# Kernel optimization log

Hardware: AMD Instinct MI355X
Metric: run time of the kernel (lower is better)

## Reference

```python
import jax, jax.numpy as jnp
import numpy as np

E = 1024
H = 4
N = 4096


def _l2norm(x, eps=1e-8):
    n = jnp.linalg.norm(x, axis=-1, keepdims=True)
    return x / jnp.maximum(n, eps)


def mha(q, k, v, in_w, in_b, out_w, out_b):
    # torch nn.MultiheadAttention, unbatched (L, E) inputs, H heads
    d = E // H
    qp = q @ in_w[:E].T + in_b[:E]            # [Lq, E]
    kp = k @ in_w[E:2 * E].T + in_b[E:2 * E]  # [Lk, E]
    vp = v @ in_w[2 * E:].T + in_b[2 * E:]    # [Lk, E]
    qh = qp.reshape(-1, H, d).transpose(1, 0, 2)  # [H, Lq, d]
    kh = kp.reshape(-1, H, d).transpose(1, 0, 2)
    vh = vp.reshape(-1, H, d).transpose(1, 0, 2)
    scores = jnp.einsum('hqd,hkd->hqk', qh, kh) / jnp.sqrt(jnp.asarray(d, qh.dtype))
    attn = jax.nn.softmax(scores, axis=-1)
    oh = jnp.einsum('hqk,hkd->hqd', attn, vh)     # [H, Lq, d]
    o = oh.transpose(1, 0, 2).reshape(-1, E)
    return o @ out_w.T + out_b


def setup_inputs() -> dict:
    key = jax.random.key(0)
    ks = jax.random.split(key, 20)
    f = lambda k, shape, s=1.0: jax.random.normal(k, shape, dtype=jnp.float32) * s
    inp = {
        'local_feat': _l2norm(f(ks[0], (N, E))),
        'global_feat': _l2norm(f(ks[1], (N, E))),
        'text_feat': _l2norm(f(ks[2], (N, E))),
        'pos_emb_local': f(ks[3], (E,), E ** -0.5),
        'pos_emb_global': f(ks[4], (E,), E ** -0.5),
        'fc_w': f(ks[5], (E, E), 0.02), 'fc_b': f(ks[6], (E,), 0.02),
        'lg_in_w': f(ks[7], (3 * E, E), 0.02), 'lg_in_b': f(ks[8], (3 * E,), 0.02),
        'lg_out_w': f(ks[9], (E, E), 0.02), 'lg_out_b': f(ks[10], (E,), 0.02),
        'vt_in_w': f(ks[11], (3 * E, E), 0.02), 'vt_in_b': f(ks[12], (3 * E,), 0.02),
        'vt_out_w': f(ks[13], (E, E), 0.02), 'vt_out_b': f(ks[14], (E,), 0.02),
        'ml_in_w': f(ks[15], (3 * E, E), 0.02), 'ml_in_b': f(ks[16], (3 * E,), 0.02),
        'ml_out_w': f(ks[17], (E, E), 0.02), 'ml_out_b': f(ks[18], (E,), 0.02),
        'quantity': 512,
    }
    return inp


def reference(local_feat, global_feat, text_feat, pos_emb_local, pos_emb_global,
              fc_w, fc_b, lg_in_w, lg_in_b, lg_out_w, lg_out_b,
              vt_in_w, vt_in_b, vt_out_w, vt_out_b,
              ml_in_w, ml_in_b, ml_out_w, ml_out_b, quantity):
    lf = local_feat + pos_emb_local
    gf = global_feat + pos_emb_global
    # local_global
    local_global = mha(lf, gf, gf, lg_in_w, lg_in_b, lg_out_w, lg_out_b) + lf
    # fusion_fc on text (applied fresh in textual_local, textual_global, repeat_text)
    tf = text_feat @ fc_w.T + fc_b
    # textual_local / textual_global (shared fusion_visual_textual weights)
    text_local = mha(tf, lf, lf, vt_in_w, vt_in_b, vt_out_w, vt_out_b) + lf
    text_global = mha(tf, gf, gf, vt_in_w, vt_in_b, vt_out_w, vt_out_b) + tf
    # middle_layer fusions (shared weights)
    gt_gl = mha(local_global, text_global, text_global, ml_in_w, ml_in_b, ml_out_w, ml_out_b)
    gl_lt = mha(text_local, local_global, local_global, ml_in_w, ml_in_b, ml_out_w, ml_out_b)
    full = mha(gl_lt, gt_gl, gt_gl, ml_in_w, ml_in_b, ml_out_w, ml_out_b)
    fusion = mha(tf, full, full, ml_in_w, ml_in_b, ml_out_w, ml_out_b) * tf
    # per-sample cosine-similarity matrices (batched replacement of the .item() loops)
    Q = quantity
    B = N // Q
    ff = _l2norm(fusion.reshape(B, Q, E))
    lb = _l2norm(local_feat.reshape(B, Q, E))
    logits = jnp.einsum('bqe,bke->bqk', ff, lb)  # [B, Q, Q]
    return logits
```

## Files before the change

kernel.cpp:

```cpp
#include <hip/hip_runtime.h>
#include <hip/hip_bf16.h>


typedef __attribute__((ext_vector_type(8))) short short8;
typedef __attribute__((ext_vector_type(4))) float f32x4;
typedef unsigned long long ull;
typedef long long ll;

namespace {
constexpr int NTOK = 4096;
constexpr int EMB  = 1024;
constexpr int QTY  = 512;
}

__device__ __forceinline__ float bf2f(unsigned short u) {
    union { float f; unsigned int i; } x; x.i = ((unsigned int)u) << 16; return x.f;
}
__device__ __forceinline__ unsigned short f2bf(float f) {
    union { float f; unsigned int i; } x; x.f = f;
    unsigned int r = x.i + 0x7fffu + ((x.i >> 16) & 1u);
    return (unsigned short)(r >> 16);
}

#define GLOAD_LDS16(g, l) __builtin_amdgcn_global_load_lds( \
    (const __attribute__((address_space(1))) void*)(g),     \
    (__attribute__((address_space(3))) void*)(l), 16, 0, 0)

template<int SPLITS, int OUTM>
__global__ __launch_bounds__(256)
void gemm_mfma(const unsigned short* __restrict__ Ah, const unsigned short* __restrict__ Al,
               int lda, ll sAz,
               const unsigned short* __restrict__ Bh, const unsigned short* __restrict__ Bl,
               int ldb, ll sBz,
               void* __restrict__ Cp, void* __restrict__ Clp,
               int ldc, ll sCz,
               int K, float alpha, const float* __restrict__ bias, int biasRow,
               const unsigned short* __restrict__ resH, const unsigned short* __restrict__ resL,
               ll sRz, int resMode)
{
    constexpr int NTILES = (SPLITS == 3 ? 4 : (SPLITS == 2 ? 3 : 2));
    constexpr int TSZ = 128 * 32;
    __shared__ unsigned short lds[NTILES * TSZ];
    const int tid  = threadIdx.x;
    const int brow = blockIdx.y * 128;
    const int bcol = blockIdx.x * 128;
    const ll   z   = blockIdx.z;
    Ah += z * sAz; Bh += z * sBz;
    if constexpr (SPLITS == 3) Al += z * sAz;
    if constexpr (SPLITS >= 2) Bl += z * sBz;

    const int lane = tid & 63;
    const int wv = tid >> 6, wr = wv >> 1, wc = wv & 1;
    const int l15 = lane & 15, l4 = lane >> 4;

    f32x4 acc[4][4];
    #pragma unroll
    for (int m = 0; m < 4; ++m)
        #pragma unroll
        for (int n = 0; n < 4; ++n) acc[m][n] = (f32x4){0.f, 0.f, 0.f, 0.f};

    for (int k0 = 0; k0 < K; k0 += 32) {
        #pragma unroll
        for (int i = 0; i < 2; ++i) {
            int idx = tid + i * 256;
            int row = idx >> 2;
            int kc  = (idx & 3) ^ ((row >> 1) & 3);
            GLOAD_LDS16(Ah + (ull)(brow + row) * lda + k0 + kc * 8, &lds[idx * 8]);
            GLOAD_LDS16(Bh + (ull)(bcol + row) * ldb + k0 + kc * 8, &lds[TSZ + idx * 8]);
            if constexpr (SPLITS >= 2)
                GLOAD_LDS16(Bl + (ull)(bcol + row) * ldb + k0 + kc * 8, &lds[2 * TSZ + idx * 8]);
            if constexpr (SPLITS == 3)
                GLOAD_LDS16(Al + (ull)(brow + row) * lda + k0 + kc * 8, &lds[3 * TSZ + idx * 8]);
        }
        __syncthreads();

        short8 ah[4], bh[4], bl2[4], al2[4];
        #pragma unroll
        for (int m = 0; m < 4; ++m) {
            int rr = wr * 64 + m * 16 + l15;
            int sl = l4 ^ ((rr >> 1) & 3);
            int off = rr * 32 + sl * 8;
            ah[m] = *(const short8*)&lds[off];
            if constexpr (SPLITS == 3) al2[m] = *(const short8*)&lds[3 * TSZ + off];
        }
        #pragma unroll
        for (int n = 0; n < 4; ++n) {
            int rr = wc * 64 + n * 16 + l15;
            int sl = l4 ^ ((rr >> 1) & 3);
            int off = rr * 32 + sl * 8;
            bh[n] = *(const short8*)&lds[TSZ + off];
            if constexpr (SPLITS >= 2) bl2[n] = *(const short8*)&lds[2 * TSZ + off];
        }
        #pragma unroll
        for (int m = 0; m < 4; ++m)
            #pragma unroll
            for (int n = 0; n < 4; ++n) {
                acc[m][n] = __builtin_amdgcn_mfma_f32_16x16x32_bf16(ah[m], bh[n], acc[m][n], 0, 0, 0);
                if constexpr (SPLITS >= 2)
                    acc[m][n] = __builtin_amdgcn_mfma_f32_16x16x32_bf16(ah[m], bl2[n], acc[m][n], 0, 0, 0);
                if constexpr (SPLITS == 3)
                    acc[m][n] = __builtin_amdgcn_mfma_f32_16x16x32_bf16(al2[m], bh[n], acc[m][n], 0, 0, 0);
            }
        __syncthreads();
    }

    float* Cf = (float*)Cp + z * sCz;
    unsigned short* Ch = (unsigned short*)Cp + z * sCz;
    unsigned short* Cl = (unsigned short*)Clp + z * sCz;
    const unsigned short* rH = resH + z * sRz;
    const unsigned short* rL = resL + z * sRz;
    const int rowB = brow + wr * 64 + l4 * 4;
    const int colB = bcol + wc * 64 + l15;
    #pragma unroll
    for (int n = 0; n < 4; ++n) {
        int col = colB + n * 16;
        #pragma unroll
        for (int m = 0; m < 4; ++m) {
            #pragma unroll
            for (int r = 0; r < 4; ++r) {
                int row = rowB + m * 16 + r;
                ull ci = (ull)row * ldc + col;
                float v = acc[m][n][r] * alpha;
                if (bias) v += biasRow ? bias[row] : bias[col];
                if (resMode == 1)      v += bf2f(rH[ci]) + bf2f(rL[ci]);
                else if (resMode == 2) v *= bf2f(rH[ci]) + bf2f(rL[ci]);
                if constexpr (OUTM == 0)      Cf[ci] = v;
                else if constexpr (OUTM == 1) Ch[ci] = f2bf(v);
                else {
                    unsigned short h = f2bf(v);
                    Ch[ci] = h;
                    Cl[ci] = f2bf(v - bf2f(h));
                }
            }
        }
    }
}

__global__ __launch_bounds__(256)
void gemm_qkproj(const unsigned short* a0, const unsigned short* a1,
                 const unsigned short* a2, const unsigned short* a3,
                 const unsigned short* __restrict__ W,
                 unsigned short* __restrict__ QK,
                 const float* __restrict__ bias)
{
    constexpr int TSZ = 128 * 32;
    __shared__ unsigned short lds[2 * TSZ];
    const int tid  = threadIdx.x;
    const int brow = blockIdx.y * 128;
    const int bcol = blockIdx.x * 128;
    const int z = blockIdx.z;
    const int j = z & 1, bb = z >> 1;
    const unsigned short* Ah = (z == 0) ? a0 : (z == 1) ? a1 : (z == 2) ? a2 : a3;
    const unsigned short* Bh = W + (ull)j * EMB * EMB;
    unsigned short* C = QK + (ull)bb * NTOK * 2048 + j * 1024;
    const float* bi = bias + j * 1024;

    const int lane = tid & 63;
    const int wv = tid >> 6, wr = wv >> 1, wc = wv & 1;
    const int l15 = lane & 15, l4 = lane >> 4;

    f32x4 acc[4][4];
    #pragma unroll
    for (int m = 0; m < 4; ++m)
        #pragma unroll
        for (int n = 0; n < 4; ++n) acc[m][n] = (f32x4){0.f, 0.f, 0.f, 0.f};

    for (int k0 = 0; k0 < EMB; k0 += 32) {
        #pragma unroll
        for (int i = 0; i < 2; ++i) {
            int idx = tid + i * 256;
            int row = idx >> 2;
            int kc  = (idx & 3) ^ ((row >> 1) & 3);
            GLOAD_LDS16(Ah + (ull)(brow + row) * EMB + k0 + kc * 8, &lds[idx * 8]);
            GLOAD_LDS16(Bh + (ull)(bcol + row) * EMB + k0 + kc * 8, &lds[TSZ + idx * 8]);
        }
        __syncthreads();

        short8 ah[4], bh[4];
        #pragma unroll
        for (int m = 0; m < 4; ++m) {
            int rr = wr * 64 + m * 16 + l15;
            int sl = l4 ^ ((rr >> 1) & 3);
            ah[m] = *(const short8*)&lds[rr * 32 + sl * 8];
        }
        #pragma unroll
        for (int n = 0; n < 4; ++n) {
            int rr = wc * 64 + n * 16 + l15;
            int sl = l4 ^ ((rr >> 1) & 3);
            bh[n] = *(const short8*)&lds[TSZ + rr * 32 + sl * 8];
        }
        #pragma unroll
        for (int m = 0; m < 4; ++m)
            #pragma unroll
            for (int n = 0; n < 4; ++n)
                acc[m][n] = __builtin_amdgcn_mfma_f32_16x16x32_bf16(ah[m], bh[n], acc[m][n], 0, 0, 0);
        __syncthreads();
    }

    const int rowB = brow + wr * 64 + l4 * 4;
    const int colB = bcol + wc * 64 + l15;
    #pragma unroll
    for (int n = 0; n < 4; ++n) {
        int col = colB + n * 16;
        float bv = bi[col];
        #pragma unroll
        for (int m = 0; m < 4; ++m)
            #pragma unroll
            for (int r = 0; r < 4; ++r) {
                int row = rowB + m * 16 + r;
                C[(ull)row * 2048 + col] = f2bf(acc[m][n][r] + bv);
            }
    }
}

template<int NSPLIT>
__global__ __launch_bounds__(512)
void flash_attn(const unsigned short* __restrict__ QK,
                const unsigned short* __restrict__ VT,
                unsigned short* __restrict__ Opart, float* __restrict__ ml,
                unsigned short* __restrict__ attH)
{
    constexpr int KVB = 64;
    constexpr int NTILE = (NTOK / NSPLIT) / KVB;
    __shared__ unsigned short Kt[2][KVB * 256];
    __shared__ unsigned short Vt[2][256 * KVB];

    const int tid = threadIdx.x;
    const int w = tid >> 6, lane = tid & 63;
    const int l15 = lane & 15, l4 = lane >> 4;
    const int bid = blockIdx.x;
    const int zz = bid & 7, qt = bid >> 3;
    const int h = zz & 3;
    int b, sp;
    if constexpr (NSPLIT == 2) { b = 0; sp = zz >> 2; }
    else                       { b = zz >> 2; sp = 0; }
    const int qrow = qt * 128 + w * 16 + l15;
    const int kv0 = sp * (NTOK / NSPLIT);
    const unsigned short* QKb = QK + (ull)b * NTOK * 2048;
    const unsigned short* VTb = VT + (ull)b * 1024 * 4096;

    short8 qreg[8];
    {
        const unsigned short* qp = QKb + (ull)qrow * 2048 + h * 256;
        #pragma unroll
        for (int c = 0; c < 8; ++c) {
            short8 x = *(const short8*)&qp[c * 32 + l4 * 8];
            #pragma unroll
            for (int j = 0; j < 8; ++j)
                x[j] = (short)f2bf(bf2f((unsigned short)x[j]) * 0.0625f);
            qreg[c] = x;
        }
    }

    f32x4 oacc[16];
    #pragma unroll
    for (int dn = 0; dn < 16; ++dn) oacc[dn] = (f32x4){0.f, 0.f, 0.f, 0.f};
    float m_r = -1e30f, l_r = 0.f;

    auto stage = [&](int t, int buf) {
        int base = kv0 + t * KVB;
        #pragma unroll
        for (int i = 0; i < 4; ++i) {
            int s = tid + i * 512;
            int r = s >> 5, c = s & 31;
            int c0 = c ^ (r & 7);
            GLOAD_LDS16(QKb + (ull)(base + r) * 2048 + 1024 + h * 256 + c0 * 8,
                        &Kt[buf][s * 8]);
        }
        #pragma unroll
        for (int i = 0; i < 4; ++i) {
            int s = tid + i * 512;
            int r = s >> 3, c = s & 7;
            int c0 = c ^ (r & 7);
            GLOAD_LDS16(VTb + (ull)(h * 256 + r) * 4096 + base + c0 * 8,
                        &Vt[buf][s * 8]);
        }
    };

    stage(0, 0);
    for (int t = 0; t < NTILE; ++t) {
        if (t + 1 < NTILE) {
            stage(t + 1, (t + 1) & 1);
            asm volatile("s_waitcnt vmcnt(8)");
        } else {
            asm volatile("s_waitcnt vmcnt(0)");
        }
        __builtin_amdgcn_s_barrier();

        const unsigned short* Kb = Kt[t & 1];
        const unsigned short* Vb = Vt[t & 1];

        f32x4 sacc[4];
        #pragma unroll
        for (int fk = 0; fk < 4; ++fk) sacc[fk] = (f32x4){0.f, 0.f, 0.f, 0.f};
        #pragma unroll
        for (int fk = 0; fk < 4; ++fk) {
            int r = fk * 16 + l15;
            int rx = r & 7;
            #pragma unroll
            for (int c = 0; c < 8; ++c) {
                int ch = (4 * c + l4) ^ rx;
                short8 kf = *(const short8*)&Kb[r * 256 + ch * 8];
                sacc[fk] = __builtin_amdgcn_mfma_f32_16x16x32_bf16(kf, qreg[c], sacc[fk], 0, 0, 0);
            }
        }

        float tm = sacc[0][0];
        #pragma unroll
        for (int fk = 0; fk < 4; ++fk)
            #pragma unroll
            for (int rr = 0; rr < 4; ++rr) tm = fmaxf(tm, sacc[fk][rr]);
        tm = fmaxf(tm, __shfl_xor(tm, 16));
        tm = fmaxf(tm, __shfl_xor(tm, 32));

        bool nomax = __all(tm <= m_r + 5.545f);
        if (!nomax) {
            float mnew = fmaxf(m_r, tm);
            float corr = __expf(m_r - mnew);
            float c4[4];
            #pragma unroll
            for (int r = 0; r < 4; ++r) c4[r] = __shfl(corr, l4 * 4 + r);
            #pragma unroll
            for (int dn = 0; dn < 16; ++dn)
                #pragma unroll
                for (int r = 0; r < 4; ++r) oacc[dn][r] *= c4[r];
            l_r *= corr;
            m_r = mnew;
        }

        float p[16]; float ls = 0.f;
        #pragma unroll
        for (int fk = 0; fk < 4; ++fk)
            #pragma unroll
            for (int rr = 0; rr < 4; ++rr) {
                float e = __expf(sacc[fk][rr] - m_r);
                p[fk * 4 + rr] = e; ls += e;
            }
        ls += __shfl_xor(ls, 16);
        ls += __shfl_xor(ls, 32);
        l_r += ls;

        unsigned int W[4][2];
        #pragma unroll
        for (int f = 0; f < 4; ++f)
            #pragma unroll
            for (int pp = 0; pp < 2; ++pp)
                W[f][pp] = (unsigned int)f2bf(p[f * 4 + 2 * pp]) |
                           ((unsigned int)f2bf(p[f * 4 + 2 * pp + 1]) << 16);

        const int sbase = l15 + ((l4 & 1) << 5);
        const bool hi = (l4 >> 1) & 1;
        #pragma unroll
        for (int kvc = 0; kvc < 2; ++kvc) {
            unsigned int a0 = (unsigned int)__shfl((int)W[2 * kvc][0], sbase);
            unsigned int a1 = (unsigned int)__shfl((int)W[2 * kvc][1], sbase);
            unsigned int a2 = (unsigned int)__shfl((int)W[2 * kvc][0], sbase + 16);
            unsigned int a3 = (unsigned int)__shfl((int)W[2 * kvc][1], sbase + 16);
            unsigned int b0 = (unsigned int)__shfl((int)W[2 * kvc + 1][0], sbase);
            unsigned int b1 = (unsigned int)__shfl((int)W[2 * kvc + 1][1], sbase);
            unsigned int b2 = (unsigned int)__shfl((int)W[2 * kvc + 1][0], sbase + 16);
            unsigned int b3 = (unsigned int)__shfl((int)W[2 * kvc + 1][1], sbase + 16);
            union { unsigned int u[4]; short8 s8; } pa;
            pa.u[0] = hi ? b0 : a0; pa.u[1] = hi ? b1 : a1;
            pa.u[2] = hi ? b2 : a2; pa.u[3] = hi ? b3 : a3;

            #pragma unroll
            for (int dn = 0; dn < 16; ++dn) {
                int row = dn * 16 + l15;
                int ch = (kvc * 4 + l4) ^ (row & 7);
                short8 vf = *(const short8*)&Vb[row * 64 + ch * 8];
                oacc[dn] = __builtin_amdgcn_mfma_f32_16x16x32_bf16(pa.s8, vf, oacc[dn], 0, 0, 0);
            }
        }
        __builtin_amdgcn_s_barrier();
    }

    float inv = 1.f / l_r;
    float i4[4];
    #pragma unroll
    for (int r = 0; r < 4; ++r) i4[r] = __shfl(inv, l4 * 4 + r);

    if constexpr (NSPLIT == 2) {
        unsigned short* Ob = Opart + (((ull)b * 2 + sp) * 4 + h) * NTOK * 256;
        #pragma unroll
        for (int dn = 0; dn < 16; ++dn) {
            int d = dn * 16 + l15;
            #pragma unroll
            for (int r = 0; r < 4; ++r) {
                int q = qt * 128 + w * 16 + l4 * 4 + r;
                Ob[(ull)q * 256 + d] = f2bf(oacc[dn][r] * i4[r]);
            }
        }
        if (l4 == 0) {
            float2* mlp = (float2*)ml + (((ull)b * 2 + sp) * 4 + h) * NTOK + qrow;
            *mlp = make_float2(m_r, l_r);
        }
    } else {
        unsigned short* Ob = attH + (ull)b * NTOK * EMB;
        #pragma unroll
        for (int dn = 0; dn < 16; ++dn) {
            int d = dn * 16 + l15;
            #pragma unroll
            for (int r = 0; r < 4; ++r) {
                int q = qt * 128 + w * 16 + l4 * 4 + r;
                Ob[(ull)q * EMB + h * 256 + d] = f2bf(oacc[dn][r] * i4[r]);
            }
        }
    }
}

__global__ __launch_bounds__(256)
void flash_combine(const unsigned short* __restrict__ Opart, const float* __restrict__ ml,
                   unsigned short* __restrict__ attH)
{
    const int bx = blockIdx.x;
    const int b = bx >> 12, q = bx & 4095;
    const int t = threadIdx.x;
    const int h = t >> 6, d4 = (t & 63) * 4;

    float2 m0 = ((const float2*)ml)[(((ull)b * 2 + 0) * 4 + h) * NTOK + q];
    float2 m1 = ((const float2*)ml)[(((ull)b * 2 + 1) * 4 + h) * NTOK + q];
    float ms = fmaxf(m0.x, m1.x);
    float w0 = __expf(m0.x - ms) * m0.y;
    float w1 = __expf(m1.x - ms) * m1.y;
    float inv = 1.f / (w0 + w1);
    w0 *= inv; w1 *= inv;

    ushort4 o0 = *(const ushort4*)&Opart[((((ull)b * 2 + 0) * 4 + h) * NTOK + q) * 256 + d4];
    ushort4 o1 = *(const ushort4*)&Opart[((((ull)b * 2 + 1) * 4 + h) * NTOK + q) * 256 + d4];
    ushort4 ho;
    ho.x = f2bf(w0 * bf2f(o0.x) + w1 * bf2f(o1.x));
    ho.y = f2bf(w0 * bf2f(o0.y) + w1 * bf2f(o1.y));
    ho.z = f2bf(w0 * bf2f(o0.z) + w1 * bf2f(o1.z));
    ho.w = f2bf(w0 * bf2f(o0.w) + w1 * bf2f(o1.w));
    *(ushort4*)&attH[(ull)b * NTOK * EMB + (ull)q * EMB + h * 256 + d4] = ho;
}

template<bool F32IN>
__global__ __launch_bounds__(256)
void l2norm_rows(const float* __restrict__ inF, const unsigned short* __restrict__ inH,
                 const unsigned short* __restrict__ inL,
                 unsigned short* __restrict__ oH, unsigned short* __restrict__ oL)
{
    const ull row = blockIdx.x;
    const int t = threadIdx.x;
    const int lane = t & 63, wid = t >> 6;
    __shared__ float red[4];

    float v[4];
    if constexpr (F32IN) {
        float4 x = *(const float4*)&inF[row * EMB + t * 4];
        v[0] = x.x; v[1] = x.y; v[2] = x.z; v[3] = x.w;
    } else {
        ushort4 hh = *(const ushort4*)&inH[row * EMB + t * 4];
        ushort4 ll2 = *(const ushort4*)&inL[row * EMB + t * 4];
        v[0] = bf2f(hh.x) + bf2f(ll2.x); v[1] = bf2f(hh.y) + bf2f(ll2.y);
        v[2] = bf2f(hh.z) + bf2f(ll2.z); v[3] = bf2f(hh.w) + bf2f(ll2.w);
    }
    float ss = v[0] * v[0] + v[1] * v[1] + v[2] * v[2] + v[3] * v[3];
    #pragma unroll
    for (int o = 32; o > 0; o >>= 1) ss += __shfl_down(ss, o);
    if (lane == 0) red[wid] = ss;
    __syncthreads();
    ss = red[0] + red[1] + red[2] + red[3];

    float inv = 1.f / fmaxf(sqrtf(ss), 1e-8f);
    ushort4 ho, lo;
    float s0 = v[0] * inv, s1 = v[1] * inv, s2 = v[2] * inv, s3 = v[3] * inv;
    ho.x = f2bf(s0); lo.x = f2bf(s0 - bf2f(ho.x));
    ho.y = f2bf(s1); lo.y = f2bf(s1 - bf2f(ho.y));
    ho.z = f2bf(s2); lo.z = f2bf(s2 - bf2f(ho.z));
    ho.w = f2bf(s3); lo.w = f2bf(s3 - bf2f(ho.w));
    *(ushort4*)&oH[row * EMB + t * 4] = ho;
    *(ushort4*)&oL[row * EMB + t * 4] = lo;
}

__global__ __launch_bounds__(256)
void add_pos_pair(const float* __restrict__ in, const float* __restrict__ pos,
                  unsigned short* __restrict__ oH, unsigned short* __restrict__ oL)
{
    ull i = ((ull)blockIdx.x * 256 + threadIdx.x) * 4;
    float4 a = *(const float4*)&in[i];
    float4 p = *(const float4*)&pos[(int)(i & (EMB - 1))];
    float w[4] = { a.x + p.x, a.y + p.y, a.z + p.z, a.w + p.w };
    ushort4 ho, lo;
    ho.x = f2bf(w[0]); lo.x = f2bf(w[0] - bf2f(ho.x));
    ho.y = f2bf(w[1]); lo.y = f2bf(w[1] - bf2f(ho.y));
    ho.z = f2bf(w[2]); lo.z = f2bf(w[2] - bf2f(ho.z));
    ho.w = f2bf(w[3]); lo.w = f2bf(w[3] - bf2f(ho.w));
    *(ushort4*)&oH[i] = ho;
    *(ushort4*)&oL[i] = lo;
}

__global__ __launch_bounds__(256)
void split_pair(const float* __restrict__ in, unsigned short* __restrict__ oH,
                unsigned short* __restrict__ oL)
{
    ull i = ((ull)blockIdx.x * 256 + threadIdx.x) * 4;
    float4 a = *(const float4*)&in[i];
    float w[4] = { a.x, a.y, a.z, a.w };
    ushort4 ho, lo;
    ho.x = f2bf(w[0]); lo.x = f2bf(w[0] - bf2f(ho.x));
    ho.y = f2bf(w[1]); lo.y = f2bf(w[1] - bf2f(ho.y));
    ho.z = f2bf(w[2]); lo.z = f2bf(w[2] - bf2f(ho.z));
    ho.w = f2bf(w[3]); lo.w = f2bf(w[3] - bf2f(ho.w));
    *(ushort4*)&oH[i] = ho;
    *(ushort4*)&oL[i] = lo;
}

__global__ __launch_bounds__(256)
void cast_bf16(const float* __restrict__ in, unsigned short* __restrict__ out)
{
    ull i = ((ull)blockIdx.x * 256 + threadIdx.x) * 4;
    float4 a = *(const float4*)&in[i];
    ushort4 ho;
    ho.x = f2bf(a.x); ho.y = f2bf(a.y); ho.z = f2bf(a.z); ho.w = f2bf(a.w);
    *(ushort4*)&out[i] = ho;
}

namespace {

template<int S, int O>
inline void G(dim3 grid,
              const unsigned short* Ah, const unsigned short* Al, int lda, ll sAz,
              const unsigned short* Bh, const unsigned short* Bl, int ldb, ll sBz,
              void* Ch, void* Cl, int ldc, ll sCz,
              int K, float alpha, const float* bias, int biasRow,
              const unsigned short* rh, const unsigned short* rl, ll sRz, int rm,
              hipStream_t st)
{
    gemm_mfma<S, O><<<grid, dim3(256), 0, st>>>(Ah, Al, lda, sAz, Bh, Bl, ldb, sBz,
                                                Ch, Cl, ldc, sCz, K, alpha, bias, biasRow,
                                                rh, rl, sRz, rm);
}

struct Bufs {
    unsigned short *Ph[6], *Pl[6];
    unsigned short *ATTh, *QK, *VT, *Wih, *Woh, *Wol, *Opart;
    float *ml;
};

void run_mha(int batch,
             const unsigned short* qh, ll sQ,
             const unsigned short* kh, ll sK,
             const float* in_w, const float* in_b,
             const float* out_w, const float* out_b,
             unsigned short* dsth, unsigned short* dstl,
             const unsigned short* resh, const unsigned short* resl, ll sR, int resMode,
             const Bufs& B, bool convW, hipStream_t s)
{
    const ull EE = (ull)EMB * EMB;
    const ll  TE = (ll)NTOK * EMB;
    const ll  VTBS = (ll)1024 * 4096;
    if (convW) {
        cast_bf16<<<3 * EE / 1024, 256, 0, s>>>(in_w, B.Wih);
        split_pair<<<EE / 1024, 256, 0, s>>>(out_w, B.Woh, B.Wol);
    }
    gemm_qkproj<<<dim3(8, 32, 2 * batch), 256, 0, s>>>(
        qh, kh, qh + sQ, kh + sK, B.Wih, B.QK, in_b);
    G<1, 1>(dim3(32, 8, batch), B.Wih + 2 * EE, nullptr, EMB, 0, kh, nullptr, EMB, sK,
            B.VT, nullptr, 4096, VTBS, EMB, 1.f, in_b + 2 * EMB, 1, nullptr, nullptr, 0, 0, s);

    if (batch == 1) {
        flash_attn<2><<<256, 512, 0, s>>>(B.QK, B.VT, B.Opart, B.ml, B.ATTh);
        flash_combine<<<NTOK, 256, 0, s>>>(B.Opart, B.ml, B.ATTh);
    } else {
        flash_attn<1><<<256, 512, 0, s>>>(B.QK, B.VT, B.Opart, B.ml, B.ATTh);
    }

    G<2, 2>(dim3(8, 32, batch), B.ATTh, nullptr, EMB, TE, B.Woh, B.Wol, EMB, 0,
            dsth, dstl, EMB, 2 * TE, EMB, 1.f, out_b, 0, resh, resl, sR, resMode, s);
}

}

extern "C" void kernel_launch(void* const* d_in, const int* in_sizes, int n_in,
                              void* d_out, int out_size, void* d_ws, size_t ws_size,
                              hipStream_t stream) {
    const float* local_feat  = (const float*)d_in[0];
    const float* global_feat = (const float*)d_in[1];
    const float* text_feat   = (const float*)d_in[2];
    const float* pos_l       = (const float*)d_in[3];
    const float* pos_g       = (const float*)d_in[4];
    const float* fc_w        = (const float*)d_in[5];
    const float* fc_b        = (const float*)d_in[6];
    const float* lg_in_w     = (const float*)d_in[7];
    const float* lg_in_b     = (const float*)d_in[8];
    const float* lg_out_w    = (const float*)d_in[9];
    const float* lg_out_b    = (const float*)d_in[10];
    const float* vt_in_w     = (const float*)d_in[11];
    const float* vt_in_b     = (const float*)d_in[12];
    const float* vt_out_w    = (const float*)d_in[13];
    const float* vt_out_b    = (const float*)d_in[14];
    const float* ml_in_w     = (const float*)d_in[15];
    const float* ml_in_b     = (const float*)d_in[16];
    const float* ml_out_w    = (const float*)d_in[17];
    const float* ml_out_b    = (const float*)d_in[18];
    float* out = (float*)d_out;

    const ull TE = (ull)NTOK * EMB;
    const ull EE = (ull)EMB * EMB;
    unsigned short* w = (unsigned short*)d_ws;
    Bufs B;
    for (int i = 0; i < 6; ++i) { B.Ph[i] = w + (2 * i) * TE; B.Pl[i] = w + (2 * i + 1) * TE; }
    B.ATTh  = w + 12 * TE;
    B.QK    = w + 14 * TE;
    B.VT    = w + 18 * TE;
    B.Opart = w + 20 * TE;
    B.ml    = (float*)(w + 24 * TE);
    B.Wih   = w + 25 * TE;
    B.Woh   = B.Wih + 3 * EE;
    B.Wol   = B.Woh + EE;

    add_pos_pair<<<TE / 1024, 256, 0, stream>>>(local_feat, pos_l, B.Ph[0], B.Pl[0]);
    add_pos_pair<<<TE / 1024, 256, 0, stream>>>(global_feat, pos_g, B.Ph[1], B.Pl[1]);

    split_pair<<<TE / 1024, 256, 0, stream>>>(text_feat, B.QK, B.QK + TE);
    split_pair<<<EE / 1024, 256, 0, stream>>>(fc_w, B.Woh, B.Wol);
    G<3, 2>(dim3(EMB / 128, NTOK / 128), B.QK, B.QK + TE, EMB, 0, B.Woh, B.Wol, EMB, 0,
            B.Ph[2], B.Pl[2], EMB, 0, EMB, 1.f, fc_b, 0, nullptr, nullptr, 0, 0, stream);

    const ll T2 = (ll)2 * TE, T4 = (ll)4 * TE;
    run_mha(1, B.Ph[0], 0, B.Ph[1], 0, lg_in_w, lg_in_b, lg_out_w, lg_out_b,
            B.Ph[3], B.Pl[3], B.Ph[0], B.Pl[0], 0, 1, B, true, stream);
    run_mha(2, B.Ph[2], 0, B.Ph[0], T2, vt_in_w, vt_in_b, vt_out_w, vt_out_b,
            B.Ph[4], B.Pl[4], B.Ph[0], B.Pl[0], T4, 1, B, true, stream);
    run_mha(2, B.Ph[3], T2, B.Ph[5], -T4, ml_in_w, ml_in_b, ml_out_w, ml_out_b,
            B.Ph[0], B.Pl[0], nullptr, nullptr, 0, 0, B, true, stream);
    run_mha(1, B.Ph[1], 0, B.Ph[0], 0, ml_in_w, ml_in_b, ml_out_w, ml_out_b,
            B.Ph[3], B.Pl[3], nullptr, nullptr, 0, 0, B, false, stream);
    run_mha(1, B.Ph[2], 0, B.Ph[3], 0, ml_in_w, ml_in_b, ml_out_w, ml_out_b,
            B.Ph[4], B.Pl[4], B.Ph[2], B.Pl[2], 0, 2, B, false, stream);

    l2norm_rows<false><<<NTOK, 256, 0, stream>>>(nullptr, B.Ph[4], B.Pl[4], B.Ph[4], B.Pl[4]);
    l2norm_rows<true ><<<NTOK, 256, 0, stream>>>(local_feat, nullptr, nullptr, B.Ph[5], B.Pl[5]);

    G<3, 0>(dim3(QTY / 128, QTY / 128, 8),
            B.Ph[4], B.Pl[4], EMB, (ll)QTY * EMB,
            B.Ph[5], B.Pl[5], EMB, (ll)QTY * EMB,
            out, nullptr, QTY, (ll)QTY * QTY,
            EMB, 1.f, nullptr, 0, nullptr, nullptr, 0, 0, stream);
}
```

Baseline: 1.685 ms.

## Batch local_global and textual MHAs into shared grouped projection, attention, and output launches

The first three independent attention blocks (local_global, textual_local, textual_global) now run together. Grouped GEMM kernels compute all six Q/K projections and three V projections, then one flash-attention launch covers 12 head/batch groups without KV splitting, and one fused output projection adds the residual. Fewer launches and larger grids should fill the GPU better than two separate MHA passes. The cost is more workspace and losing the split-KV path for the single-batch case, and the workspace layout is reshuffled, which risks buffer overlaps.

```diff
diff --git a/kernel.cpp b/kernel.cpp
--- a/kernel.cpp
+++ b/kernel.cpp
@@ -175,7 +175,6 @@
             GLOAD_LDS16(Bh + (ull)(bcol + row) * EMB + k0 + kc * 8, &lds[TSZ + idx * 8]);
         }
         __syncthreads();
-
         short8 ah[4], bh[4];
         #pragma unroll
         for (int m = 0; m < 4; ++m) {
@@ -213,7 +212,250 @@
     }
 }
 
-template<int NSPLIT>
+__global__ __launch_bounds__(256)
+void gemm_proj6(const unsigned short* a0, const unsigned short* a1,
+                const unsigned short* a2, const unsigned short* a3,
+                const unsigned short* a4, const unsigned short* a5,
+                const unsigned short* __restrict__ w0, const unsigned short* __restrict__ w1,
+                const float* __restrict__ b0, const float* __restrict__ b1,
+                unsigned short* __restrict__ QK)
+{
+    constexpr int TSZ = 128 * 32;
+    __shared__ unsigned short lds[2 * TSZ];
+    const int tid  = threadIdx.x;
+    const int brow = blockIdx.y * 128;
+    const int bcol = blockIdx.x * 128;
+    const int z = blockIdx.z;
+    const int j = z & 1, m6 = z >> 1;
+    const unsigned short* Ah = (z == 0) ? a0 : (z == 1) ? a1 : (z == 2) ? a2
+                              : (z == 3) ? a3 : (z == 4) ? a4 : a5;
+    const unsigned short* Bh = ((m6 == 0) ? w0 : w1) + (ull)j * EMB * EMB;
+    unsigned short* C = QK + (ull)m6 * NTOK * 2048 + j * 1024;
+    const float* bi = ((m6 == 0) ? b0 : b1) + j * 1024;
+
+    const int lane = tid & 63;
+    const int wv = tid >> 6, wr = wv >> 1, wc = wv & 1;
+    const int l15 = lane & 15, l4 = lane >> 4;
+
+    f32x4 acc[4][4];
+    #pragma unroll
+    for (int m = 0; m < 4; ++m)
+        #pragma unroll
+        for (int n = 0; n < 4; ++n) acc[m][n] = (f32x4){0.f, 0.f, 0.f, 0.f};
+
+    for (int k0 = 0; k0 < EMB; k0 += 32) {
+        #pragma unroll
+        for (int i = 0; i < 2; ++i) {
+            int idx = tid + i * 256;
+            int row = idx >> 2;
+            int kc  = (idx & 3) ^ ((row >> 1) & 3);
+            GLOAD_LDS16(Ah + (ull)(brow + row) * EMB + k0 + kc * 8, &lds[idx * 8]);
+            GLOAD_LDS16(Bh + (ull)(bcol + row) * EMB + k0 + kc * 8, &lds[TSZ + idx * 8]);
+        }
+        __syncthreads();
+        short8 ah[4], bh[4];
+        #pragma unroll
+        for (int m = 0; m < 4; ++m) {
+            int rr = wr * 64 + m * 16 + l15;
+            int sl = l4 ^ ((rr >> 1) & 3);
+            ah[m] = *(const short8*)&lds[rr * 32 + sl * 8];
+        }
+        #pragma unroll
+        for (int n = 0; n < 4; ++n) {
+            int rr = wc * 64 + n * 16 + l15;
+            int sl = l4 ^ ((rr >> 1) & 3);
+            bh[n] = *(const short8*)&lds[TSZ + rr * 32 + sl * 8];
+        }
+        #pragma unroll
+        for (int m = 0; m < 4; ++m)
+            #pragma unroll
+            for (int n = 0; n < 4; ++n)
+                acc[m][n] = __builtin_amdgcn_mfma_f32_16x16x32_bf16(ah[m], bh[n], acc[m][n], 0, 0, 0);
+        __syncthreads();
+    }
+
+    const int rowB = brow + wr * 64 + l4 * 4;
+    const int colB = bcol + wc * 64 + l15;
+    #pragma unroll
+    for (int n = 0; n < 4; ++n) {
+        int col = colB + n * 16;
+        float bv = bi[col];
+        #pragma unroll
+        for (int m = 0; m < 4; ++m)
+            #pragma unroll
+            for (int r = 0; r < 4; ++r) {
+                int row = rowB + m * 16 + r;
+                C[(ull)row * 2048 + col] = f2bf(acc[m][n][r] + bv);
+            }
+    }
+}
+
+__global__ __launch_bounds__(256)
+void gemm_vt3(const unsigned short* f0, const unsigned short* f1,
+              const unsigned short* f2,
+              const unsigned short* __restrict__ w0, const unsigned short* __restrict__ w1,
+              const float* __restrict__ b0, const float* __restrict__ b1,
+              unsigned short* __restrict__ VT)
+{
+    constexpr int TSZ = 128 * 32;
+    __shared__ unsigned short lds[2 * TSZ];
+    const int tid  = threadIdx.x;
+    const int brow = blockIdx.y * 128;
+    const int bcol = blockIdx.x * 128;
+    const int z = blockIdx.z;
+    const unsigned short* Ah = ((z == 0) ? w0 : w1) + 2ull * EMB * EMB;
+    const unsigned short* Bh = (z == 0) ? f0 : (z == 1) ? f1 : f2;
+    const float* bi = ((z == 0) ? b0 : b1) + 2048;
+    unsigned short* C = VT + (ull)z * 1024 * 4096;
+
+    const int lane = tid & 63;
+    const int wv = tid >> 6, wr = wv >> 1, wc = wv & 1;
+    const int l15 = lane & 15, l4 = lane >> 4;
+
+    f32x4 acc[4][4];
+    #pragma unroll
+    for (int m = 0; m < 4; ++m)
+        #pragma unroll
+        for (int n = 0; n < 4; ++n) acc[m][n] = (f32x4){0.f, 0.f, 0.f, 0.f};
+
+    for (int k0 = 0; k0 < EMB; k0 += 32) {
+        #pragma unroll
+        for (int i = 0; i < 2; ++i) {
+            int idx = tid + i * 256;
+            int row = idx >> 2;
+            int kc  = (idx & 3) ^ ((row >> 1) & 3);
+            GLOAD_LDS16(Ah + (ull)(brow + row) * EMB + k0 + kc * 8, &lds[idx * 8]);
+            GLOAD_LDS16(Bh + (ull)(bcol + row) * EMB + k0 + kc * 8, &lds[TSZ + idx * 8]);
+        }
+        __syncthreads();
+        short8 ah[4], bh[4];
+        #pragma unroll
+        for (int m = 0; m < 4; ++m) {
+            int rr = wr * 64 + m * 16 + l15;
+            int sl = l4 ^ ((rr >> 1) & 3);
+            ah[m] = *(const short8*)&lds[rr * 32 + sl * 8];
+        }
+        #pragma unroll
+        for (int n = 0; n < 4; ++n) {
+            int rr = wc * 64 + n * 16 + l15;
+            int sl = l4 ^ ((rr >> 1) & 3);
+            bh[n] = *(const short8*)&lds[TSZ + rr * 32 + sl * 8];
+        }
+        #pragma unroll
+        for (int m = 0; m < 4; ++m)
+            #pragma unroll
+            for (int n = 0; n < 4; ++n)
+                acc[m][n] = __builtin_amdgcn_mfma_f32_16x16x32_bf16(ah[m], bh[n], acc[m][n], 0, 0, 0);
+        __syncthreads();
+    }
+
+    const int rowB = brow + wr * 64 + l4 * 4;
+    const int colB = bcol + wc * 64 + l15;
+    #pragma unroll
+    for (int n = 0; n < 4; ++n) {
+        int col = colB + n * 16;
+        #pragma unroll
+        for (int m = 0; m < 4; ++m)
+            #pragma unroll
+            for (int r = 0; r < 4; ++r) {
+                int row = rowB + m * 16 + r;
+                C[(ull)row * 4096 + col] = f2bf(acc[m][n][r] + bi[row]);
+            }
+    }
+}
+
+__global__ __launch_bounds__(256)
+void gemm_out3(const unsigned short* __restrict__ ATTh,
+               const unsigned short* __restrict__ w0h, const unsigned short* __restrict__ w0l,
+               const unsigned short* __restrict__ w1h, const unsigned short* __restrict__ w1l,
+               const float* __restrict__ b0, const float* __restrict__ b1,
+               unsigned short* __restrict__ dsth, unsigned short* __restrict__ dstl,
+               const unsigned short* r0h, const unsigned short* r0l,
+               const unsigned short* r1h, const unsigned short* r1l,
+               const unsigned short* r2h, const unsigned short* r2l)
+{
+    constexpr int TSZ = 128 * 32;
+    __shared__ unsigned short lds[3 * TSZ];
+    const int tid  = threadIdx.x;
+    const int brow = blockIdx.y * 128;
+    const int bcol = blockIdx.x * 128;
+    const int z = blockIdx.z;
+    const ll TE = (ll)NTOK * EMB;
+    const unsigned short* Ah = ATTh + z * TE;
+    const unsigned short* Bh = (z == 0) ? w0h : w1h;
+    const unsigned short* Bl = (z == 0) ? w0l : w1l;
+    const float* bi = (z == 0) ? b0 : b1;
+    unsigned short* Ch = dsth + z * 2 * TE;
+    unsigned short* Cl = dstl + z * 2 * TE;
+    const unsigned short* rH = (z == 0) ? r0h : (z == 1) ? r1h : r2h;
+    const unsigned short* rL = (z == 0) ? r0l : (z == 1) ? r1l : r2l;
+
+    const int lane = tid & 63;
+    const int wv = tid >> 6, wr = wv >> 1, wc = wv & 1;
+    const int l15 = lane & 15, l4 = lane >> 4;
+
+    f32x4 acc[4][4];
+    #pragma unroll
+    for (int m = 0; m < 4; ++m)
+        #pragma unroll
+        for (int n = 0; n < 4; ++n) acc[m][n] = (f32x4){0.f, 0.f, 0.f, 0.f};
+
+    for (int k0 = 0; k0 < EMB; k0 += 32) {
+        #pragma unroll
+        for (int i = 0; i < 2; ++i) {
+            int idx = tid + i * 256;
+            int row = idx >> 2;
+            int kc  = (idx & 3) ^ ((row >> 1) & 3);
+            GLOAD_LDS16(Ah + (ull)(brow + row) * EMB + k0 + kc * 8, &lds[idx * 8]);
+            GLOAD_LDS16(Bh + (ull)(bcol + row) * EMB + k0 + kc * 8, &lds[TSZ + idx * 8]);
+            GLOAD_LDS16(Bl + (ull)(bcol + row) * EMB + k0 + kc * 8, &lds[2 * TSZ + idx * 8]);
+        }
+        __syncthreads();
+        short8 ah[4], bh[4], bl2[4];
+        #pragma unroll
+        for (int m = 0; m < 4; ++m) {
+            int rr = wr * 64 + m * 16 + l15;
+            int sl = l4 ^ ((rr >> 1) & 3);
+            ah[m] = *(const short8*)&lds[rr * 32 + sl * 8];
+        }
+        #pragma unroll
+        for (int n = 0; n < 4; ++n) {
+            int rr = wc * 64 + n * 16 + l15;
+            int sl = l4 ^ ((rr >> 1) & 3);
+            bh[n]  = *(const short8*)&lds[TSZ + rr * 32 + sl * 8];
+            bl2[n] = *(const short8*)&lds[2 * TSZ + rr * 32 + sl * 8];
+        }
+        #pragma unroll
+        for (int m = 0; m < 4; ++m)
+            #pragma unroll
+            for (int n = 0; n < 4; ++n) {
+                acc[m][n] = __builtin_amdgcn_mfma_f32_16x16x32_bf16(ah[m], bh[n], acc[m][n], 0, 0, 0);
+                acc[m][n] = __builtin_amdgcn_mfma_f32_16x16x32_bf16(ah[m], bl2[n], acc[m][n], 0, 0, 0);
+            }
+        __syncthreads();
+    }
+
+    const int rowB = brow + wr * 64 + l4 * 4;
+    const int colB = bcol + wc * 64 + l15;
+    #pragma unroll
+    for (int n = 0; n < 4; ++n) {
+        int col = colB + n * 16;
+        float bv = bi[col];
+        #pragma unroll
+        for (int m = 0; m < 4; ++m)
+            #pragma unroll
+            for (int r = 0; r < 4; ++r) {
+                int row = rowB + m * 16 + r;
+                ull ci = (ull)row * EMB + col;
+                float v = acc[m][n][r] + bv + bf2f(rH[ci]) + bf2f(rL[ci]);
+                unsigned short h = f2bf(v);
+                Ch[ci] = h;
+                Cl[ci] = f2bf(v - bf2f(h));
+            }
+    }
+}
+
+template<int NSPLIT, int NZ>
 __global__ __launch_bounds__(512)
 void flash_attn(const unsigned short* __restrict__ QK,
                 const unsigned short* __restrict__ VT,
@@ -229,7 +471,7 @@
     const int w = tid >> 6, lane = tid & 63;
     const int l15 = lane & 15, l4 = lane >> 4;
     const int bid = blockIdx.x;
-    const int zz = bid & 7, qt = bid >> 3;
+    const int zz = bid % NZ, qt = bid / NZ;
     const int h = zz & 3;
     int b, sp;
     if constexpr (NSPLIT == 2) { b = 0; sp = zz >> 2; }
@@ -536,7 +778,8 @@
 
 struct Bufs {
     unsigned short *Ph[6], *Pl[6];
-    unsigned short *ATTh, *QK, *VT, *Wih, *Woh, *Wol, *Opart;
+    unsigned short *ATTh, *QK, *VT, *Opart;
+    unsigned short *Wih0, *Wih1, *Wo0h, *Wo0l, *Wo1h, *Wo1l;
     float *ml;
 };
 
@@ -553,22 +796,22 @@
     const ll  TE = (ll)NTOK * EMB;
     const ll  VTBS = (ll)1024 * 4096;
     if (convW) {
-        cast_bf16<<<3 * EE / 1024, 256, 0, s>>>(in_w, B.Wih);
-        split_pair<<<EE / 1024, 256, 0, s>>>(out_w, B.Woh, B.Wol);
+        cast_bf16<<<3 * EE / 1024, 256, 0, s>>>(in_w, B.Wih0);
+        split_pair<<<EE / 1024, 256, 0, s>>>(out_w, B.Wo0h, B.Wo0l);
     }
     gemm_qkproj<<<dim3(8, 32, 2 * batch), 256, 0, s>>>(
-        qh, kh, qh + sQ, kh + sK, B.Wih, B.QK, in_b);
-    G<1, 1>(dim3(32, 8, batch), B.Wih + 2 * EE, nullptr, EMB, 0, kh, nullptr, EMB, sK,
+        qh, kh, qh + sQ, kh + sK, B.Wih0, B.QK, in_b);
+    G<1, 1>(dim3(32, 8, batch), B.Wih0 + 2 * EE, nullptr, EMB, 0, kh, nullptr, EMB, sK,
             B.VT, nullptr, 4096, VTBS, EMB, 1.f, in_b + 2 * EMB, 1, nullptr, nullptr, 0, 0, s);
 
     if (batch == 1) {
-        flash_attn<2><<<256, 512, 0, s>>>(B.QK, B.VT, B.Opart, B.ml, B.ATTh);
+        flash_attn<2, 8><<<256, 512, 0, s>>>(B.QK, B.VT, B.Opart, B.ml, B.ATTh);
         flash_combine<<<NTOK, 256, 0, s>>>(B.Opart, B.ml, B.ATTh);
     } else {
-        flash_attn<1><<<256, 512, 0, s>>>(B.QK, B.VT, B.Opart, B.ml, B.ATTh);
-    }
-
-    G<2, 2>(dim3(8, 32, batch), B.ATTh, nullptr, EMB, TE, B.Woh, B.Wol, EMB, 0,
+        flash_attn<1, 8><<<256, 512, 0, s>>>(B.QK, B.VT, B.Opart, B.ml, B.ATTh);
+    }
+
+    G<2, 2>(dim3(8, 32, batch), B.ATTh, nullptr, EMB, TE, B.Wo0h, B.Wo0l, EMB, 0,
             dsth, dstl, EMB, 2 * TE, EMB, 1.f, out_b, 0, resh, resl, sR, resMode, s);
 }
 
@@ -604,27 +847,41 @@
     Bufs B;
     for (int i = 0; i < 6; ++i) { B.Ph[i] = w + (2 * i) * TE; B.Pl[i] = w + (2 * i + 1) * TE; }
     B.ATTh  = w + 12 * TE;
-    B.QK    = w + 14 * TE;
-    B.VT    = w + 18 * TE;
-    B.Opart = w + 20 * TE;
+    B.QK    = w + 15 * TE;
+    B.Opart = B.QK + 2 * TE;
+    B.VT    = w + 21 * TE;
     B.ml    = (float*)(w + 24 * TE);
-    B.Wih   = w + 25 * TE;
-    B.Woh   = B.Wih + 3 * EE;
-    B.Wol   = B.Woh + EE;
+    B.Wih0  = w + 24 * TE + 131072;
+    B.Wih1  = B.Wih0 + 3 * EE;
+    B.Wo0h  = B.Wih1 + 3 * EE;
+    B.Wo0l  = B.Wo0h + EE;
+    B.Wo1h  = B.Wo0l + EE;
+    B.Wo1l  = B.Wo1h + EE;
 
     add_pos_pair<<<TE / 1024, 256, 0, stream>>>(local_feat, pos_l, B.Ph[0], B.Pl[0]);
     add_pos_pair<<<TE / 1024, 256, 0, stream>>>(global_feat, pos_g, B.Ph[1], B.Pl[1]);
 
     split_pair<<<TE / 1024, 256, 0, stream>>>(text_feat, B.QK, B.QK + TE);
-    split_pair<<<EE / 1024, 256, 0, stream>>>(fc_w, B.Woh, B.Wol);
-    G<3, 2>(dim3(EMB / 128, NTOK / 128), B.QK, B.QK + TE, EMB, 0, B.Woh, B.Wol, EMB, 0,
+    split_pair<<<EE / 1024, 256, 0, stream>>>(fc_w, B.Wo0h, B.Wo0l);
+    G<3, 2>(dim3(EMB / 128, NTOK / 128), B.QK, B.QK + TE, EMB, 0, B.Wo0h, B.Wo0l, EMB, 0,
             B.Ph[2], B.Pl[2], EMB, 0, EMB, 1.f, fc_b, 0, nullptr, nullptr, 0, 0, stream);
 
+    cast_bf16<<<3 * EE / 1024, 256, 0, stream>>>(lg_in_w, B.Wih0);
+    cast_bf16<<<3 * EE / 1024, 256, 0, stream>>>(vt_in_w, B.Wih1);
+    split_pair<<<EE / 1024, 256, 0, stream>>>(lg_out_w, B.Wo0h, B.Wo0l);
+    split_pair<<<EE / 1024, 256, 0, stream>>>(vt_out_w, B.Wo1h, B.Wo1l);
+    gemm_proj6<<<dim3(8, 32, 6), 256, 0, stream>>>(
+        B.Ph[0], B.Ph[1], B.Ph[2], B.Ph[0], B.Ph[2], B.Ph[1],
+        B.Wih0, B.Wih1, lg_in_b, vt_in_b, B.QK);
+    gemm_vt3<<<dim3(32, 8, 3), 256, 0, stream>>>(
+        B.Ph[1], B.Ph[0], B.Ph[1], B.Wih0, B.Wih1, lg_in_b, vt_in_b, B.VT);
+    flash_attn<1, 12><<<384, 512, 0, stream>>>(B.QK, B.VT, nullptr, nullptr, B.ATTh);
+    gemm_out3<<<dim3(8, 32, 3), 256, 0, stream>>>(
+        B.ATTh, B.Wo0h, B.Wo0l, B.Wo1h, B.Wo1l, lg_out_b, vt_out_b,
+        B.Ph[3], B.Pl[3],
+        B.Ph[0], B.Pl[0], B.Ph[0], B.Pl[0], B.Ph[2], B.Pl[2]);
+
     const ll T2 = (ll)2 * TE, T4 = (ll)4 * TE;
-    run_mha(1, B.Ph[0], 0, B.Ph[1], 0, lg_in_w, lg_in_b, lg_out_w, lg_out_b,
-            B.Ph[3], B.Pl[3], B.Ph[0], B.Pl[0], 0, 1, B, true, stream);
-    run_mha(2, B.Ph[2], 0, B.Ph[0], T2, vt_in_w, vt_in_b, vt_out_w, vt_out_b,
-            B.Ph[4], B.Pl[4], B.Ph[0], B.Pl[0], T4, 1, B, true, stream);
     run_mha(2, B.Ph[3], T2, B.Ph[5], -T4, ml_in_w, ml_in_b, ml_out_w, ml_out_b,
             B.Ph[0], B.Pl[0], nullptr, nullptr, 0, 0, B, true, stream);
     run_mha(1, B.Ph[1], 0, B.Ph[0], 0, ml_in_w, ml_in_b, ml_out_w, ml_out_b,
```

New measurement: 1.668 ms. About the same (-1.0%).
